# Optimization experiments

Hardware: AMD Instinct MI355X
Metric: run time of the kernel (lower is better)

## Reference

```python
import jax, jax.numpy as jnp
import numpy as np

B, S, HID = 2, 2048, 2048
H, HKV, DH = 32, 8, 64
GROUPS = H // HKV
SCALE = DH ** -0.5
ROPE_THETA = 10000.0
NEG_INF = jnp.finfo(jnp.float32).min


def setup_inputs() -> dict:
    key = jax.random.key(0)
    ks = jax.random.split(key, 6)
    hidden_states = jax.random.normal(ks[0], (B, S, HID), dtype=jnp.float32)
    # true rotary embeddings (HF Llama style): inv_freq over half dim, duplicated
    inv_freq = 1.0 / (ROPE_THETA ** (np.arange(0, DH, 2, dtype=np.float32) / DH))
    freqs = np.arange(S, dtype=np.float32)[:, None] * inv_freq[None, :]  # [S, DH/2]
    emb = np.concatenate([freqs, freqs], axis=-1)                        # [S, DH]
    cos = jnp.broadcast_to(jnp.asarray(np.cos(emb), jnp.float32), (B, S, DH))
    sin = jnp.broadcast_to(jnp.asarray(np.sin(emb), jnp.float32), (B, S, DH))
    # additive causal mask [1,1,S,S]
    causal = jnp.tril(jnp.ones((S, S), dtype=bool))
    attention_mask = jnp.where(causal, 0.0, NEG_INF)[None, None].astype(jnp.float32)
    std = 0.02
    Wq = jax.random.normal(ks[1], (H * DH, HID), dtype=jnp.float32) * std
    Wk = jax.random.normal(ks[2], (HKV * DH, HID), dtype=jnp.float32) * std
    Wv = jax.random.normal(ks[3], (HKV * DH, HID), dtype=jnp.float32) * std
    Wo = jax.random.normal(ks[4], (HID, H * DH), dtype=jnp.float32) * std
    return {"hidden_states": hidden_states, "cos": cos, "sin": sin,
            "attention_mask": attention_mask, "Wq": Wq, "Wk": Wk, "Wv": Wv, "Wo": Wo}


def _rotate_half(x):
    x1, x2 = jnp.split(x, 2, axis=-1)
    return jnp.concatenate([-x2, x1], axis=-1)


def reference(hidden_states, cos, sin, attention_mask, Wq, Wk, Wv, Wo):
    b, s, _ = hidden_states.shape
    # projections -> [B, H(kv), S, DH]
    q = (hidden_states @ Wq.T).reshape(b, s, H, DH).transpose(0, 2, 1, 3)
    k = (hidden_states @ Wk.T).reshape(b, s, HKV, DH).transpose(0, 2, 1, 3)
    v = (hidden_states @ Wv.T).reshape(b, s, HKV, DH).transpose(0, 2, 1, 3)
    # RoPE (cos/sin: [B,S,DH] -> broadcast over head axis)
    c = cos[:, None, :, :]
    sn = sin[:, None, :, :]
    q = q * c + _rotate_half(q) * sn
    k = k * c + _rotate_half(k) * sn
    # GQA: repeat kv heads
    k = jnp.repeat(k, GROUPS, axis=1)  # [B,H,S,DH]
    v = jnp.repeat(v, GROUPS, axis=1)
    # eager attention: full [B,H,S,S] scores in memory
    scores = jnp.einsum('bhqd,bhkd->bhqk', q, k) * SCALE + attention_mask[:, :, :, :s]
    attn = jax.nn.softmax(scores, axis=-1)
    out = jnp.einsum('bhqk,bhkd->bhqd', attn, v)
    out = out.transpose(0, 2, 1, 3).reshape(b, s, H * DH)
    return out @ Wo.T
```

## Files before the change

### kernel.cpp

```cpp
#include <hip/hip_runtime.h>
#include <hip/hip_bf16.h>
#include <cstdint>
#include <cstddef>

#define B_    2
#define S_    2048
#define HID_  2048
#define H_    32
#define HKV_  8
#define DH_   64
#define SC2_  0.1803368801111244f

typedef __bf16 bf16;
typedef bf16  bf16x2 __attribute__((ext_vector_type(2)));
typedef bf16  bf16x4 __attribute__((ext_vector_type(4)));
typedef bf16  bf16x8 __attribute__((ext_vector_type(8)));
typedef float f32x4  __attribute__((ext_vector_type(4)));
typedef float f32x16 __attribute__((ext_vector_type(16)));
typedef uint32_t u32x2 __attribute__((ext_vector_type(2)));

typedef __attribute__((address_space(3))) uint32_t  lds_u32_t;
typedef __attribute__((address_space(1))) const uint32_t glob_u32_t;

__device__ __forceinline__ void async16(const void* g, void* l) {
    __builtin_amdgcn_global_load_lds((glob_u32_t*)g, (lds_u32_t*)l, 16, 0, 0);
}

__device__ __forceinline__ bf16x8 cvt8(float4 a, float4 b) {
    bf16x8 r;
    r[0] = (bf16)a.x; r[1] = (bf16)a.y; r[2] = (bf16)a.z; r[3] = (bf16)a.w;
    r[4] = (bf16)b.x; r[5] = (bf16)b.y; r[6] = (bf16)b.z; r[7] = (bf16)b.w;
    return r;
}

__device__ __forceinline__ uint32_t pkbf(float a, float b) {
    bf16x2 t; t[0] = (bf16)a; t[1] = (bf16)b;
    return __builtin_bit_cast(uint32_t, t);
}
__device__ __forceinline__ bf16x8 mk8(uint32_t a, uint32_t b, uint32_t c, uint32_t d) {
    union { uint32_t u[4]; bf16x8 v; } t;
    t.u[0] = a; t.u[1] = b; t.u[2] = c; t.u[3] = d;
    return t.v;
}

__global__ __launch_bounds__(256) void cvt_all_kernel(
    const float* __restrict__ X,  const float* __restrict__ Wq,
    const float* __restrict__ Wk, const float* __restrict__ Wv,
    const float* __restrict__ Wo,
    bf16* __restrict__ Xb,  bf16* __restrict__ Wqb, bf16* __restrict__ Wkb,
    bf16* __restrict__ Wvb, bf16* __restrict__ Wob)
{
    const int i = blockIdx.x * 256 + threadIdx.x;
    const float* src; bf16* dst; int off;
    if (i < 1048576)      { src = X;  dst = Xb;  off = i; }
    else if (i < 1572864) { src = Wq; dst = Wqb; off = i - 1048576; }
    else if (i < 1703936) { src = Wk; dst = Wkb; off = i - 1572864; }
    else if (i < 1835008) { src = Wv; dst = Wvb; off = i - 1703936; }
    else                  { src = Wo; dst = Wob; off = i - 1835008; }
    float4 a = ((const float4*)src)[2 * off];
    float4 b = ((const float4*)src)[2 * off + 1];
    ((bf16x8*)dst)[off] = cvt8(a, b);
}

__global__ __launch_bounds__(256) void gemm_qkv_kernel(
    const bf16* __restrict__ A,
    const bf16* __restrict__ Wqb, const bf16* __restrict__ Wkb,
    const bf16* __restrict__ Wvb,
    const float* __restrict__ cs, const float* __restrict__ sn,
    bf16* __restrict__ Qo, bf16* __restrict__ Ko, bf16* __restrict__ Vt)
{
    __shared__ bf16 a_lds[2][128 * 64];
    __shared__ bf16 b_lds[2][128 * 64];

    const int tid  = threadIdx.x;
    const int wave = tid >> 6;
    const int lane = tid & 63;
    const int quad = lane >> 4;
    const int l16  = lane & 15;
    const int wm   = wave >> 1;
    const int wn   = wave & 1;

    const int idx = blockIdx.x + 32 * blockIdx.y;
    const int swz = (idx & 7) * 96 + (idx >> 3);
    const int m0  = (swz & 31) * 128;
    const int n0  = (swz >> 5) * 128;

    f32x4 acc[4][4];
    #pragma unroll
    for (int mt = 0; mt < 4; ++mt)
        #pragma unroll
        for (int nt = 0; nt < 4; ++nt)
            acc[mt][nt] = (f32x4){0.f, 0.f, 0.f, 0.f};

    int srow[4], sgcol[4];
    const bf16* browp[4];
    #pragma unroll
    for (int i = 0; i < 4; ++i) {
        const int e = tid * 8 + i * 2048;
        srow[i] = e >> 6;
        const int chunk = (e >> 3) & 7;
        sgcol[i] = (chunk ^ (srow[i] & 7)) << 3;
        const int n = n0 + srow[i];
        browp[i] = (n < 2048) ? (Wqb + (size_t)n * HID_)
                 : (n < 2560) ? (Wkb + (size_t)(n - 2048) * HID_)
                              : (Wvb + (size_t)(n - 2560) * HID_);
    }

    #pragma unroll
    for (int i = 0; i < 4; ++i) {
        async16(A + (size_t)(m0 + srow[i]) * HID_ + sgcol[i],
                &a_lds[0][tid * 8 + i * 2048]);
        async16(browp[i] + sgcol[i],
                &b_lds[0][tid * 8 + i * 2048]);
    }
    __syncthreads();

    for (int k0 = 0; k0 < HID_; k0 += 64) {
        const int cur = (k0 >> 6) & 1;
        if (k0 + 64 < HID_) {
            #pragma unroll
            for (int i = 0; i < 4; ++i) {
                async16(A + (size_t)(m0 + srow[i]) * HID_ + k0 + 64 + sgcol[i],
                        &a_lds[cur ^ 1][tid * 8 + i * 2048]);
                async16(browp[i] + k0 + 64 + sgcol[i],
                        &b_lds[cur ^ 1][tid * 8 + i * 2048]);
            }
        }
        const bf16* al = a_lds[cur];
        const bf16* bl = b_lds[cur];
        #pragma unroll
        for (int ks = 0; ks < 2; ++ks) {
            bf16x8 af[4], bfr[4];
            #pragma unroll
            for (int mt = 0; mt < 4; ++mt) {
                const int row = wm * 64 + mt * 16 + l16;
                const int c = (ks * 4 + quad) ^ (row & 7);
                af[mt] = *(const bf16x8*)(&al[row * 64 + c * 8]);
            }
            #pragma unroll
            for (int nt = 0; nt < 4; ++nt) {
                const int row = wn * 64 + nt * 16 + l16;
                const int c = (ks * 4 + quad) ^ (row & 7);
                bfr[nt] = *(const bf16x8*)(&bl[row * 64 + c * 8]);
            }
            #pragma unroll
            for (int mt = 0; mt < 4; ++mt)
                #pragma unroll
                for (int nt = 0; nt < 4; ++nt)
                    acc[mt][nt] = __builtin_amdgcn_mfma_f32_16x16x32_bf16(
                        af[mt], bfr[nt], acc[mt][nt], 0, 0, 0);
        }
        __syncthreads();
    }

    const int nw = n0 + wn * 64;
    const int d  = l16;
    #pragma unroll
    for (int mt = 0; mt < 4; ++mt) {
        #pragma unroll
        for (int r = 0; r < 4; ++r) {
            const int m  = m0 + wm * 64 + mt * 16 + quad * 4 + r;
            const int bb = m >> 11;
            const int ss = m & (S_ - 1);
            const float v0 = acc[mt][0][r], v1 = acc[mt][1][r];
            const float v2 = acc[mt][2][r], v3 = acc[mt][3][r];
            if (nw < 2048) {
                const int h = nw >> 6;
                bf16* dp = Qo + ((size_t)(bb * H_ + h) * S_ + ss) * DH_;
                const float* cp = cs + ((size_t)bb * S_ + ss) * DH_;
                const float* sp = sn + ((size_t)bb * S_ + ss) * DH_;
                dp[ 0 + d] = (bf16)((v0 * cp[ 0 + d] - v2 * sp[ 0 + d]) * SC2_);
                dp[16 + d] = (bf16)((v1 * cp[16 + d] - v3 * sp[16 + d]) * SC2_);
                dp[32 + d] = (bf16)((v2 * cp[32 + d] + v0 * sp[32 + d]) * SC2_);
                dp[48 + d] = (bf16)((v3 * cp[48 + d] + v1 * sp[48 + d]) * SC2_);
            } else if (nw < 2560) {
                const int h = (nw - 2048) >> 6;
                bf16* dp = Ko + ((size_t)(bb * HKV_ + h) * S_ + ss) * DH_;
                const float* cp = cs + ((size_t)bb * S_ + ss) * DH_;
                const float* sp = sn + ((size_t)bb * S_ + ss) * DH_;
                dp[ 0 + d] = (bf16)(v0 * cp[ 0 + d] - v2 * sp[ 0 + d]);
                dp[16 + d] = (bf16)(v1 * cp[16 + d] - v3 * sp[16 + d]);
                dp[32 + d] = (bf16)(v2 * cp[32 + d] + v0 * sp[32 + d]);
                dp[48 + d] = (bf16)(v3 * cp[48 + d] + v1 * sp[48 + d]);
            } else {
                const int h = (nw - 2560) >> 6;
                bf16* dp = Vt + ((size_t)(bb * HKV_ + h) * DH_) * S_ + ss;
                dp[(size_t)( 0 + d) * S_] = (bf16)v0;
                dp[(size_t)(16 + d) * S_] = (bf16)v1;
                dp[(size_t)(32 + d) * S_] = (bf16)v2;
                dp[(size_t)(48 + d) * S_] = (bf16)v3;
            }
        }
    }
}

__global__ __launch_bounds__(256) void gemm_out_kernel(
    const bf16* __restrict__ A, const bf16* __restrict__ Wb,
    float* __restrict__ Y)
{
    __shared__ bf16 a_lds[2][128 * 64];
    __shared__ bf16 b_lds[2][128 * 64];

    const int tid  = threadIdx.x;
    const int wave = tid >> 6;
    const int lane = tid & 63;
    const int quad = lane >> 4;
    const int l16  = lane & 15;
    const int wm   = wave >> 1;
    const int wn   = wave & 1;

    const int idx = blockIdx.x + 32 * blockIdx.y;
    const int swz = (idx & 7) * 64 + (idx >> 3);
    const int m0  = (swz & 31) * 128;
    const int n0  = (swz >> 5) * 128;

    f32x4 acc[4][4];
    #pragma unroll
    for (int mt = 0; mt < 4; ++mt)
        #pragma unroll
        for (int nt = 0; nt < 4; ++nt)
            acc[mt][nt] = (f32x4){0.f, 0.f, 0.f, 0.f};

    int srow[4], sgcol[4];
    #pragma unroll
    for (int i = 0; i < 4; ++i) {
        const int e = tid * 8 + i * 2048;
        srow[i] = e >> 6;
        const int chunk = (e >> 3) & 7;
        sgcol[i] = (chunk ^ (srow[i] & 7)) << 3;
    }

    #pragma unroll
    for (int i = 0; i < 4; ++i) {
        async16(A + (size_t)(m0 + srow[i]) * HID_ + sgcol[i],
                &a_lds[0][tid * 8 + i * 2048]);
        async16(Wb + (size_t)(n0 + srow[i]) * HID_ + sgcol[i],
                &b_lds[0][tid * 8 + i * 2048]);
    }
    __syncthreads();

    for (int k0 = 0; k0 < HID_; k0 += 64) {
        const int cur = (k0 >> 6) & 1;
        if (k0 + 64 < HID_) {
            #pragma unroll
            for (int i = 0; i < 4; ++i) {
                async16(A + (size_t)(m0 + srow[i]) * HID_ + k0 + 64 + sgcol[i],
                        &a_lds[cur ^ 1][tid * 8 + i * 2048]);
                async16(Wb + (size_t)(n0 + srow[i]) * HID_ + k0 + 64 + sgcol[i],
                        &b_lds[cur ^ 1][tid * 8 + i * 2048]);
            }
        }
        const bf16* al = a_lds[cur];
        const bf16* bl = b_lds[cur];
        #pragma unroll
        for (int ks = 0; ks < 2; ++ks) {
            bf16x8 af[4], bfr[4];
            #pragma unroll
            for (int mt = 0; mt < 4; ++mt) {
                const int row = wm * 64 + mt * 16 + l16;
                const int c = (ks * 4 + quad) ^ (row & 7);
                af[mt] = *(const bf16x8*)(&al[row * 64 + c * 8]);
            }
            #pragma unroll
            for (int nt = 0; nt < 4; ++nt) {
                const int row = wn * 64 + nt * 16 + l16;
                const int c = (ks * 4 + quad) ^ (row & 7);
                bfr[nt] = *(const bf16x8*)(&bl[row * 64 + c * 8]);
            }
            #pragma unroll
            for (int mt = 0; mt < 4; ++mt)
                #pragma unroll
                for (int nt = 0; nt < 4; ++nt)
                    acc[mt][nt] = __builtin_amdgcn_mfma_f32_16x16x32_bf16(
                        af[mt], bfr[nt], acc[mt][nt], 0, 0, 0);
        }
        __syncthreads();
    }

    #pragma unroll
    for (int mt = 0; mt < 4; ++mt)
        #pragma unroll
        for (int nt = 0; nt < 4; ++nt)
            #pragma unroll
            for (int r = 0; r < 4; ++r) {
                const int m = m0 + wm * 64 + mt * 16 + quad * 4 + r;
                const int n = n0 + wn * 64 + nt * 16 + l16;
                Y[(size_t)m * HID_ + n] = acc[mt][nt][r];
            }
}

__global__ __launch_bounds__(256) void attn_kernel(
    const bf16* __restrict__ Q, const bf16* __restrict__ K,
    const bf16* __restrict__ Vt, bf16* __restrict__ O)
{
    __shared__ bf16 k_lds[2][64 * 64];
    __shared__ bf16 v_lds[2][64 * 64];

    const int tid  = threadIdx.x;
    const int wave = tid >> 6;
    const int lane = tid & 63;
    const int l32  = lane & 31;
    const int half = lane >> 5;
    const int h  = blockIdx.y;
    const int b  = blockIdx.z;
    const int hkv = h >> 2;

    const bf16* Qg = Q  + (size_t)(b * H_ + h) * S_ * DH_;
    const bf16* Kg = K  + (size_t)(b * HKV_ + hkv) * S_ * DH_;
    const bf16* Vg = Vt + ((size_t)(b * HKV_ + hkv) * DH_) * S_;

    const int srow0  = tid >> 3;
    const int scolsw = ((tid & 7) ^ ((tid >> 3) & 7)) << 3;

    #pragma unroll 1
    for (int ph = 0; ph < 2; ++ph) {
        const int qt  = ph == 0 ? (int)blockIdx.x : (15 - (int)blockIdx.x);
        const int q0  = qt * 128;
        const int qb0 = q0 + wave * 32;
        const int qa  = qb0 + l32;

        bf16x8 qf[4];
        #pragma unroll
        for (int c = 0; c < 4; ++c)
            qf[c] = *(const bf16x8*)(Qg + (size_t)qa * DH_ + c * 16 + half * 8);

        f32x16 o_acc[2];
        #pragma unroll
        for (int dt = 0; dt < 2; ++dt)
            #pragma unroll
            for (int e = 0; e < 16; ++e) o_acc[dt][e] = 0.f;
        float m_i = -1e30f, l_i = 0.f;

        const int nkt = 2 * qt + 2;

        #pragma unroll
        for (int i = 0; i < 2; ++i) {
            const int row = srow0 + i * 32;
            async16(Kg + (size_t)row * DH_ + scolsw, &k_lds[0][tid * 8 + i * 2048]);
            async16(Vg + (size_t)row * S_  + scolsw, &v_lds[0][tid * 8 + i * 2048]);
        }
        __syncthreads();

        for (int kt = 0; kt < nkt; ++kt) {
            if (kt + 1 < nkt) {
                bf16* kb = k_lds[(kt + 1) & 1];
                bf16* vb = v_lds[(kt + 1) & 1];
                #pragma unroll
                for (int i = 0; i < 2; ++i) {
                    const int row = srow0 + i * 32;
                    async16(Kg + (size_t)((kt + 1) * 64 + row) * DH_ + scolsw,
                            kb + tid * 8 + i * 2048);
                    async16(Vg + (size_t)row * S_ + (kt + 1) * 64 + scolsw,
                            vb + tid * 8 + i * 2048);
                }
            }

            if (kt * 64 <= qb0 + 31) {
                const bf16* kb = k_lds[kt & 1];
                const bf16* vb = v_lds[kt & 1];
                const bool act1 = (kt * 64 + 32) <= (qb0 + 31);

                f32x16 s0, s1;
                {
                    bf16x8 kf[4];
                    #pragma unroll
                    for (int c = 0; c < 4; ++c) {
                        const int col = ((2 * c + half) ^ (l32 & 7)) << 3;
                        kf[c] = *(const bf16x8*)(kb + l32 * 64 + col);
                    }
                    f32x16 a;
                    #pragma unroll
                    for (int e = 0; e < 16; ++e) a[e] = 0.f;
                    __builtin_amdgcn_s_setprio(1);
                    #pragma unroll
                    for (int c = 0; c < 4; ++c)
                        a = __builtin_amdgcn_mfma_f32_32x32x16_bf16(kf[c], qf[c], a, 0, 0, 0);
                    __builtin_amdgcn_s_setprio(0);
                    s0 = a;
                }
                if (act1) {
                    bf16x8 kf[4];
                    #pragma unroll
                    for (int c = 0; c < 4; ++c) {
                        const int row = 32 + l32;
                        const int col = ((2 * c + half) ^ (row & 7)) << 3;
                        kf[c] = *(const bf16x8*)(kb + row * 64 + col);
                    }
                    f32x16 a;
                    #pragma unroll
                    for (int e = 0; e < 16; ++e) a[e] = 0.f;
                    __builtin_amdgcn_s_setprio(1);
                    #pragma unroll
                    for (int c = 0; c < 4; ++c)
                        a = __builtin_amdgcn_mfma_f32_32x32x16_bf16(kf[c], qf[c], a, 0, 0, 0);
                    __builtin_amdgcn_s_setprio(0);
                    s1 = a;
                }

                if (!((kt * 64 + 31) <= qb0)) {
                    const int qrel = qa - kt * 64 - 4 * half;
                    #pragma unroll
                    for (int e = 0; e < 16; ++e)
                        if (((e & 3) + 8 * (e >> 2)) > qrel) s0[e] = -1e30f;
                }
                if (act1 && !((kt * 64 + 63) <= qb0)) {
                    const int qrel = qa - kt * 64 - 32 - 4 * half;
                    #pragma unroll
                    for (int e = 0; e < 16; ++e)
                        if (((e & 3) + 8 * (e >> 2)) > qrel) s1[e] = -1e30f;
                }

                float mx = s0[0];
                #pragma unroll
                for (int e = 1; e < 16; ++e) mx = fmaxf(mx, s0[e]);
                if (act1)
                    #pragma unroll
                    for (int e = 0; e < 16; ++e) mx = fmaxf(mx, s1[e]);
                mx = fmaxf(mx, __shfl_xor(mx, 32));

                float al = 1.f;
                if (!__all(mx <= m_i + 8.f)) {
                    const float mn = fmaxf(m_i, mx);
                    al = exp2f(m_i - mn);
                    m_i = mn;
                    #pragma unroll
                    for (int dt = 0; dt < 2; ++dt)
                        #pragma unroll
                        for (int e = 0; e < 16; ++e) o_acc[dt][e] *= al;
                }

                float sm = 0.f;
                #pragma unroll
                for (int e = 0; e < 16; ++e) {
                    const float pp = exp2f(s0[e] - m_i);
                    s0[e] = pp; sm += pp;
                }
                if (act1)
                    #pragma unroll
                    for (int e = 0; e < 16; ++e) {
                        const float pp = exp2f(s1[e] - m_i);
                        s1[e] = pp; sm += pp;
                    }
                sm += __shfl_xor(sm, 32);
                l_i = l_i * al + sm;

                bf16x8 pf[4];
                {
                    uint32_t d0 = pkbf(s0[0],  s0[1]),  d1 = pkbf(s0[2],  s0[3]);
                    uint32_t d2 = pkbf(s0[4],  s0[5]),  d3 = pkbf(s0[6],  s0[7]);
                    uint32_t d4 = pkbf(s0[8],  s0[9]),  d5 = pkbf(s0[10], s0[11]);
                    uint32_t d6 = pkbf(s0[12], s0[13]), d7 = pkbf(s0[14], s0[15]);
                    u32x2 r02 = __builtin_amdgcn_permlane32_swap(d0, d2, false, false);
                    u32x2 r13 = __builtin_amdgcn_permlane32_swap(d1, d3, false, false);
                    u32x2 r46 = __builtin_amdgcn_permlane32_swap(d4, d6, false, false);
                    u32x2 r57 = __builtin_amdgcn_permlane32_swap(d5, d7, false, false);
                    pf[0] = mk8(r02[0], r13[0], r02[1], r13[1]);
                    pf[1] = mk8(r46[0], r57[0], r46[1], r57[1]);
                }
                if (act1) {
                    uint32_t d0 = pkbf(s1[0],  s1[1]),  d1 = pkbf(s1[2],  s1[3]);
                    uint32_t d2 = pkbf(s1[4],  s1[5]),  d3 = pkbf(s1[6],  s1[7]);
                    uint32_t d4 = pkbf(s1[8],  s1[9]),  d5 = pkbf(s1[10], s1[11]);
                    uint32_t d6 = pkbf(s1[12], s1[13]), d7 = pkbf(s1[14], s1[15]);
                    u32x2 r02 = __builtin_amdgcn_permlane32_swap(d0, d2, false, false);
                    u32x2 r13 = __builtin_amdgcn_permlane32_swap(d1, d3, false, false);
                    u32x2 r46 = __builtin_amdgcn_permlane32_swap(d4, d6, false, false);
                    u32x2 r57 = __builtin_amdgcn_permlane32_swap(d5, d7, false, false);
                    pf[2] = mk8(r02[0], r13[0], r02[1], r13[1]);
                    pf[3] = mk8(r46[0], r57[0], r46[1], r57[1]);
                }

                bf16x8 vf[2][4];
                #pragma unroll
                for (int dt = 0; dt < 2; ++dt)
                    #pragma unroll
                    for (int c = 0; c < 4; ++c) {
                        const int row = dt * 32 + l32;
                        const int col = ((2 * c + half) ^ (row & 7)) << 3;
                        vf[dt][c] = *(const bf16x8*)(vb + row * 64 + col);
                    }

                const int nc = act1 ? 4 : 2;
                __builtin_amdgcn_s_setprio(1);
                #pragma unroll
                for (int c = 0; c < 4; ++c) {
                    if (c >= nc) break;
                    #pragma unroll
                    for (int dt = 0; dt < 2; ++dt)
                        o_acc[dt] = __builtin_amdgcn_mfma_f32_32x32x16_bf16(
                            vf[dt][c], pf[c], o_acc[dt], 0, 0, 0);
                }
                __builtin_amdgcn_s_setprio(0);
            }
            __syncthreads();
        }

        const float inv = 1.f / l_i;
        bf16* op = O + ((size_t)(b * S_ + qa) * H_ + h) * DH_;
        #pragma unroll
        for (int dt = 0; dt < 2; ++dt)
            #pragma unroll
            for (int g = 0; g < 4; ++g) {
                bf16x4 ov;
                #pragma unroll
                for (int r = 0; r < 4; ++r) ov[r] = (bf16)(o_acc[dt][g * 4 + r] * inv);
                *(bf16x4*)(op + dt * 32 + g * 8 + half * 4) = ov;
            }
        __syncthreads();
    }
}

extern "C" void kernel_launch(void* const* d_in, const int* in_sizes, int n_in,
                              void* d_out, int out_size, void* d_ws, size_t ws_size,
                              hipStream_t stream)
{
    const float* X    = (const float*)d_in[0];
    const float* cs   = (const float*)d_in[1];
    const float* sn   = (const float*)d_in[2];
    const float* Wq   = (const float*)d_in[4];
    const float* Wk   = (const float*)d_in[5];
    const float* Wv   = (const float*)d_in[6];
    const float* Wo   = (const float*)d_in[7];
    float* Y          = (float*)d_out;

    bf16* Xb  = (bf16*)d_ws;
    bf16* Wqb = Xb  + (size_t)8388608;
    bf16* Wkb = Wqb + (size_t)4194304;
    bf16* Wvb = Wkb + (size_t)1048576;
    bf16* Wob = Wvb + (size_t)1048576;
    bf16* Qb  = Wob + (size_t)4194304;
    bf16* Kb  = Qb  + (size_t)8388608;
    bf16* Vtb = Kb  + (size_t)2097152;
    bf16* Ob  = Vtb + (size_t)2097152;

    dim3 blk(256);
    cvt_all_kernel<<<dim3(9216), blk, 0, stream>>>(X, Wq, Wk, Wv, Wo,
                                                   Xb, Wqb, Wkb, Wvb, Wob);
    gemm_qkv_kernel<<<dim3(32, 24), blk, 0, stream>>>(Xb, Wqb, Wkb, Wvb,
                                                      cs, sn, Qb, Kb, Vtb);
    attn_kernel<<<dim3(8, H_, B_), blk, 0, stream>>>(Qb, Kb, Vtb, Ob);
    gemm_out_kernel<<<dim3(32, 16), blk, 0, stream>>>(Ob, Wob, Y);
}
```

Before: 349.0 us.

## Flatten attention grid to one block per query tile with heavy-first ordering

Replaces the 512-block grid, where each block processed a pair of mirrored causal query tiles, with a 1D grid of 1024 blocks that each handle a single 128-row query tile. Blocks are ordered so the longest causal tiles (largest qt) are dispatched first across all batch-heads, then progressively shorter ones, giving a longest-job-first schedule. The aim is better load balance and more blocks in flight on the 256 CUs. The cost is losing the per-block pairing that evened out work, plus an extra Q load and prologue per tile.

```diff
diff --git a/kernel.cpp b/kernel.cpp
--- a/kernel.cpp
+++ b/kernel.cpp
@@ -301,8 +301,19 @@
     const int lane = tid & 63;
     const int l32  = lane & 31;
     const int half = lane >> 5;
-    const int h  = blockIdx.y;
-    const int b  = blockIdx.z;
+
+    const int j  = blockIdx.x;
+    const int g  = j >> 8;
+    const int p  = j & 255;
+    const int s  = p >> 6;
+    const int bh = p & 63;
+    const int h  = bh & 31;
+    const int b  = bh >> 5;
+    int qt;
+    if      (g == 0) qt = 15 - s;
+    else if (g == 1) qt = 8 + s;
+    else if (g == 2) qt = 7 - s;
+    else             qt = s;
     const int hkv = h >> 2;
 
     const bf16* Qg = Q  + (size_t)(b * H_ + h) * S_ * DH_;
@@ -312,202 +323,195 @@
     const int srow0  = tid >> 3;
     const int scolsw = ((tid & 7) ^ ((tid >> 3) & 7)) << 3;
 
-    #pragma unroll 1
-    for (int ph = 0; ph < 2; ++ph) {
-        const int qt  = ph == 0 ? (int)blockIdx.x : (15 - (int)blockIdx.x);
-        const int q0  = qt * 128;
-        const int qb0 = q0 + wave * 32;
-        const int qa  = qb0 + l32;
-
-        bf16x8 qf[4];
-        #pragma unroll
-        for (int c = 0; c < 4; ++c)
-            qf[c] = *(const bf16x8*)(Qg + (size_t)qa * DH_ + c * 16 + half * 8);
-
-        f32x16 o_acc[2];
-        #pragma unroll
-        for (int dt = 0; dt < 2; ++dt)
-            #pragma unroll
-            for (int e = 0; e < 16; ++e) o_acc[dt][e] = 0.f;
-        float m_i = -1e30f, l_i = 0.f;
-
-        const int nkt = 2 * qt + 2;
-
-        #pragma unroll
-        for (int i = 0; i < 2; ++i) {
-            const int row = srow0 + i * 32;
-            async16(Kg + (size_t)row * DH_ + scolsw, &k_lds[0][tid * 8 + i * 2048]);
-            async16(Vg + (size_t)row * S_  + scolsw, &v_lds[0][tid * 8 + i * 2048]);
-        }
-        __syncthreads();
-
-        for (int kt = 0; kt < nkt; ++kt) {
-            if (kt + 1 < nkt) {
-                bf16* kb = k_lds[(kt + 1) & 1];
-                bf16* vb = v_lds[(kt + 1) & 1];
-                #pragma unroll
-                for (int i = 0; i < 2; ++i) {
-                    const int row = srow0 + i * 32;
-                    async16(Kg + (size_t)((kt + 1) * 64 + row) * DH_ + scolsw,
-                            kb + tid * 8 + i * 2048);
-                    async16(Vg + (size_t)row * S_ + (kt + 1) * 64 + scolsw,
-                            vb + tid * 8 + i * 2048);
+    const int qb0 = qt * 128 + wave * 32;
+    const int qa  = qb0 + l32;
+    const int nkt = 2 * qt + 2;
+
+    bf16x8 qf[4];
+    #pragma unroll
+    for (int c = 0; c < 4; ++c)
+        qf[c] = *(const bf16x8*)(Qg + (size_t)qa * DH_ + c * 16 + half * 8);
+
+    f32x16 o_acc[2];
+    #pragma unroll
+    for (int dt = 0; dt < 2; ++dt)
+        #pragma unroll
+        for (int e = 0; e < 16; ++e) o_acc[dt][e] = 0.f;
+    float m_i = -1e30f, l_i = 0.f;
+
+    #pragma unroll
+    for (int i = 0; i < 2; ++i) {
+        const int row = srow0 + i * 32;
+        async16(Kg + (size_t)row * DH_ + scolsw, &k_lds[0][tid * 8 + i * 2048]);
+        async16(Vg + (size_t)row * S_  + scolsw, &v_lds[0][tid * 8 + i * 2048]);
+    }
+    __syncthreads();
+
+    for (int kt = 0; kt < nkt; ++kt) {
+        if (kt + 1 < nkt) {
+            bf16* kb = k_lds[(kt + 1) & 1];
+            bf16* vb = v_lds[(kt + 1) & 1];
+            #pragma unroll
+            for (int i = 0; i < 2; ++i) {
+                const int row = srow0 + i * 32;
+                async16(Kg + (size_t)((kt + 1) * 64 + row) * DH_ + scolsw,
+                        kb + tid * 8 + i * 2048);
+                async16(Vg + (size_t)row * S_ + (kt + 1) * 64 + scolsw,
+                        vb + tid * 8 + i * 2048);
+            }
+        }
+
+        if (kt * 64 <= qb0 + 31) {
+            const bf16* kb = k_lds[kt & 1];
+            const bf16* vb = v_lds[kt & 1];
+            const bool act1 = (kt * 64 + 32) <= (qb0 + 31);
+
+            f32x16 s0, s1;
+            {
+                bf16x8 kf[4];
+                #pragma unroll
+                for (int c = 0; c < 4; ++c) {
+                    const int col = ((2 * c + half) ^ (l32 & 7)) << 3;
+                    kf[c] = *(const bf16x8*)(kb + l32 * 64 + col);
                 }
-            }
-
-            if (kt * 64 <= qb0 + 31) {
-                const bf16* kb = k_lds[kt & 1];
-                const bf16* vb = v_lds[kt & 1];
-                const bool act1 = (kt * 64 + 32) <= (qb0 + 31);
-
-                f32x16 s0, s1;
-                {
-                    bf16x8 kf[4];
-                    #pragma unroll
-                    for (int c = 0; c < 4; ++c) {
-                        const int col = ((2 * c + half) ^ (l32 & 7)) << 3;
-                        kf[c] = *(const bf16x8*)(kb + l32 * 64 + col);
-                    }
-                    f32x16 a;
-                    #pragma unroll
-                    for (int e = 0; e < 16; ++e) a[e] = 0.f;
-                    __builtin_amdgcn_s_setprio(1);
-                    #pragma unroll
-                    for (int c = 0; c < 4; ++c)
-                        a = __builtin_amdgcn_mfma_f32_32x32x16_bf16(kf[c], qf[c], a, 0, 0, 0);
-                    __builtin_amdgcn_s_setprio(0);
-                    s0 = a;
+                f32x16 a;
+                #pragma unroll
+                for (int e = 0; e < 16; ++e) a[e] = 0.f;
+                __builtin_amdgcn_s_setprio(1);
+                #pragma unroll
+                for (int c = 0; c < 4; ++c)
+                    a = __builtin_amdgcn_mfma_f32_32x32x16_bf16(kf[c], qf[c], a, 0, 0, 0);
+                __builtin_amdgcn_s_setprio(0);
+                s0 = a;
+            }
+            if (act1) {
+                bf16x8 kf[4];
+                #pragma unroll
+                for (int c = 0; c < 4; ++c) {
+                    const int row = 32 + l32;
+                    const int col = ((2 * c + half) ^ (row & 7)) << 3;
+                    kf[c] = *(const bf16x8*)(kb + row * 64 + col);
                 }
-                if (act1) {
-                    bf16x8 kf[4];
-                    #pragma unroll
-                    for (int c = 0; c < 4; ++c) {
-                        const int row = 32 + l32;
-                        const int col = ((2 * c + half) ^ (row & 7)) << 3;
-                        kf[c] = *(const bf16x8*)(kb + row * 64 + col);
-                    }
-                    f32x16 a;
-                    #pragma unroll
-                    for (int e = 0; e < 16; ++e) a[e] = 0.f;
-                    __builtin_amdgcn_s_setprio(1);
-                    #pragma unroll
-                    for (int c = 0; c < 4; ++c)
-                        a = __builtin_amdgcn_mfma_f32_32x32x16_bf16(kf[c], qf[c], a, 0, 0, 0);
-                    __builtin_amdgcn_s_setprio(0);
-                    s1 = a;
-                }
-
-                if (!((kt * 64 + 31) <= qb0)) {
-                    const int qrel = qa - kt * 64 - 4 * half;
-                    #pragma unroll
-                    for (int e = 0; e < 16; ++e)
-                        if (((e & 3) + 8 * (e >> 2)) > qrel) s0[e] = -1e30f;
-                }
-                if (act1 && !((kt * 64 + 63) <= qb0)) {
-                    const int qrel = qa - kt * 64 - 32 - 4 * half;
-                    #pragma unroll
-                    for (int e = 0; e < 16; ++e)
-                        if (((e & 3) + 8 * (e >> 2)) > qrel) s1[e] = -1e30f;
-                }
-
-                float mx = s0[0];
-                #pragma unroll
-                for (int e = 1; e < 16; ++e) mx = fmaxf(mx, s0[e]);
-                if (act1)
-                    #pragma unroll
-                    for (int e = 0; e < 16; ++e) mx = fmaxf(mx, s1[e]);
-                mx = fmaxf(mx, __shfl_xor(mx, 32));
-
-                float al = 1.f;
-                if (!__all(mx <= m_i + 8.f)) {
-                    const float mn = fmaxf(m_i, mx);
-                    al = exp2f(m_i - mn);
-                    m_i = mn;
-                    #pragma unroll
-                    for (int dt = 0; dt < 2; ++dt)
-                        #pragma unroll
-                        for (int e = 0; e < 16; ++e) o_acc[dt][e] *= al;
-                }
-
-                float sm = 0.f;
-                #pragma unroll
-                for (int e = 0; e < 16; ++e) {
-                    const float pp = exp2f(s0[e] - m_i);
-                    s0[e] = pp; sm += pp;
-                }
-                if (act1)
-                    #pragma unroll
-                    for (int e = 0; e < 16; ++e) {
-                        const float pp = exp2f(s1[e] - m_i);
-                        s1[e] = pp; sm += pp;
-                    }
-                sm += __shfl_xor(sm, 32);
-                l_i = l_i * al + sm;
-
-                bf16x8 pf[4];
-                {
-                    uint32_t d0 = pkbf(s0[0],  s0[1]),  d1 = pkbf(s0[2],  s0[3]);
-                    uint32_t d2 = pkbf(s0[4],  s0[5]),  d3 = pkbf(s0[6],  s0[7]);
-                    uint32_t d4 = pkbf(s0[8],  s0[9]),  d5 = pkbf(s0[10], s0[11]);
-                    uint32_t d6 = pkbf(s0[12], s0[13]), d7 = pkbf(s0[14], s0[15]);
-                    u32x2 r02 = __builtin_amdgcn_permlane32_swap(d0, d2, false, false);
-                    u32x2 r13 = __builtin_amdgcn_permlane32_swap(d1, d3, false, false);
-                    u32x2 r46 = __builtin_amdgcn_permlane32_swap(d4, d6, false, false);
-                    u32x2 r57 = __builtin_amdgcn_permlane32_swap(d5, d7, false, false);
-                    pf[0] = mk8(r02[0], r13[0], r02[1], r13[1]);
-                    pf[1] = mk8(r46[0], r57[0], r46[1], r57[1]);
-                }
-                if (act1) {
-                    uint32_t d0 = pkbf(s1[0],  s1[1]),  d1 = pkbf(s1[2],  s1[3]);
-                    uint32_t d2 = pkbf(s1[4],  s1[5]),  d3 = pkbf(s1[6],  s1[7]);
-                    uint32_t d4 = pkbf(s1[8],  s1[9]),  d5 = pkbf(s1[10], s1[11]);
-                    uint32_t d6 = pkbf(s1[12], s1[13]), d7 = pkbf(s1[14], s1[15]);
-                    u32x2 r02 = __builtin_amdgcn_permlane32_swap(d0, d2, false, false);
-                    u32x2 r13 = __builtin_amdgcn_permlane32_swap(d1, d3, false, false);
-                    u32x2 r46 = __builtin_amdgcn_permlane32_swap(d4, d6, false, false);
-                    u32x2 r57 = __builtin_amdgcn_permlane32_swap(d5, d7, false, false);
-                    pf[2] = mk8(r02[0], r13[0], r02[1], r13[1]);
-                    pf[3] = mk8(r46[0], r57[0], r46[1], r57[1]);
-                }
-
-                bf16x8 vf[2][4];
+                f32x16 a;
+                #pragma unroll
+                for (int e = 0; e < 16; ++e) a[e] = 0.f;
+                __builtin_amdgcn_s_setprio(1);
+                #pragma unroll
+                for (int c = 0; c < 4; ++c)
+                    a = __builtin_amdgcn_mfma_f32_32x32x16_bf16(kf[c], qf[c], a, 0, 0, 0);
+                __builtin_amdgcn_s_setprio(0);
+                s1 = a;
+            }
+
+            if (!((kt * 64 + 31) <= qb0)) {
+                const int qrel = qa - kt * 64 - 4 * half;
+                #pragma unroll
+                for (int e = 0; e < 16; ++e)
+                    if (((e & 3) + 8 * (e >> 2)) > qrel) s0[e] = -1e30f;
+            }
+            if (act1 && !((kt * 64 + 63) <= qb0)) {
+                const int qrel = qa - kt * 64 - 32 - 4 * half;
+                #pragma unroll
+                for (int e = 0; e < 16; ++e)
+                    if (((e & 3) + 8 * (e >> 2)) > qrel) s1[e] = -1e30f;
+            }
+
+            float mx = s0[0];
+            #pragma unroll
+            for (int e = 1; e < 16; ++e) mx = fmaxf(mx, s0[e]);
+            if (act1)
+                #pragma unroll
+                for (int e = 0; e < 16; ++e) mx = fmaxf(mx, s1[e]);
+            mx = fmaxf(mx, __shfl_xor(mx, 32));
+
+            float al = 1.f;
+            if (!__all(mx <= m_i + 8.f)) {
+                const float mn = fmaxf(m_i, mx);
+                al = exp2f(m_i - mn);
+                m_i = mn;
                 #pragma unroll
                 for (int dt = 0; dt < 2; ++dt)
                     #pragma unroll
-                    for (int c = 0; c < 4; ++c) {
-                        const int row = dt * 32 + l32;
-                        const int col = ((2 * c + half) ^ (row & 7)) << 3;
-                        vf[dt][c] = *(const bf16x8*)(vb + row * 64 + col);
-                    }
-
-                const int nc = act1 ? 4 : 2;
-                __builtin_amdgcn_s_setprio(1);
+                    for (int e = 0; e < 16; ++e) o_acc[dt][e] *= al;
+            }
+
+            float sm = 0.f;
+            #pragma unroll
+            for (int e = 0; e < 16; ++e) {
+                const float pp = exp2f(s0[e] - m_i);
+                s0[e] = pp; sm += pp;
+            }
+            if (act1)
+                #pragma unroll
+                for (int e = 0; e < 16; ++e) {
+                    const float pp = exp2f(s1[e] - m_i);
+                    s1[e] = pp; sm += pp;
+                }
+            sm += __shfl_xor(sm, 32);
+            l_i = l_i * al + sm;
+
+            bf16x8 pf[4];
+            {
+                uint32_t d0 = pkbf(s0[0],  s0[1]),  d1 = pkbf(s0[2],  s0[3]);
+                uint32_t d2 = pkbf(s0[4],  s0[5]),  d3 = pkbf(s0[6],  s0[7]);
+                uint32_t d4 = pkbf(s0[8],  s0[9]),  d5 = pkbf(s0[10], s0[11]);
+                uint32_t d6 = pkbf(s0[12], s0[13]), d7 = pkbf(s0[14], s0[15]);
+                u32x2 r02 = __builtin_amdgcn_permlane32_swap(d0, d2, false, false);
+                u32x2 r13 = __builtin_amdgcn_permlane32_swap(d1, d3, false, false);
+                u32x2 r46 = __builtin_amdgcn_permlane32_swap(d4, d6, false, false);
+                u32x2 r57 = __builtin_amdgcn_permlane32_swap(d5, d7, false, false);
+                pf[0] = mk8(r02[0], r13[0], r02[1], r13[1]);
+                pf[1] = mk8(r46[0], r57[0], r46[1], r57[1]);
+            }
+            if (act1) {
+                uint32_t d0 = pkbf(s1[0],  s1[1]),  d1 = pkbf(s1[2],  s1[3]);
+                uint32_t d2 = pkbf(s1[4],  s1[5]),  d3 = pkbf(s1[6],  s1[7]);
+                uint32_t d4 = pkbf(s1[8],  s1[9]),  d5 = pkbf(s1[10], s1[11]);
+                uint32_t d6 = pkbf(s1[12], s1[13]), d7 = pkbf(s1[14], s1[15]);
+                u32x2 r02 = __builtin_amdgcn_permlane32_swap(d0, d2, false, false);
+                u32x2 r13 = __builtin_amdgcn_permlane32_swap(d1, d3, false, false);
+                u32x2 r46 = __builtin_amdgcn_permlane32_swap(d4, d6, false, false);
+                u32x2 r57 = __builtin_amdgcn_permlane32_swap(d5, d7, false, false);
+                pf[2] = mk8(r02[0], r13[0], r02[1], r13[1]);
+                pf[3] = mk8(r46[0], r57[0], r46[1], r57[1]);
+            }
+
+            bf16x8 vf[2][4];
+            #pragma unroll
+            for (int dt = 0; dt < 2; ++dt)
                 #pragma unroll
                 for (int c = 0; c < 4; ++c) {
-                    if (c >= nc) break;
-                    #pragma unroll
-                    for (int dt = 0; dt < 2; ++dt)
-                        o_acc[dt] = __builtin_amdgcn_mfma_f32_32x32x16_bf16(
-                            vf[dt][c], pf[c], o_acc[dt], 0, 0, 0);
+                    const int row = dt * 32 + l32;
+                    const int col = ((2 * c + half) ^ (row & 7)) << 3;
+                    vf[dt][c] = *(const bf16x8*)(vb + row * 64 + col);
                 }
-                __builtin_amdgcn_s_setprio(0);
-            }
-            __syncthreads();
-        }
-
-        const float inv = 1.f / l_i;
-        bf16* op = O + ((size_t)(b * S_ + qa) * H_ + h) * DH_;
-        #pragma unroll
-        for (int dt = 0; dt < 2; ++dt)
-            #pragma unroll
-            for (int g = 0; g < 4; ++g) {
-                bf16x4 ov;
-                #pragma unroll
-                for (int r = 0; r < 4; ++r) ov[r] = (bf16)(o_acc[dt][g * 4 + r] * inv);
-                *(bf16x4*)(op + dt * 32 + g * 8 + half * 4) = ov;
-            }
+
+            const int nc = act1 ? 4 : 2;
+            __builtin_amdgcn_s_setprio(1);
+            #pragma unroll
+            for (int c = 0; c < 4; ++c) {
+                if (c >= nc) break;
+                #pragma unroll
+                for (int dt = 0; dt < 2; ++dt)
+                    o_acc[dt] = __builtin_amdgcn_mfma_f32_32x32x16_bf16(
+                        vf[dt][c], pf[c], o_acc[dt], 0, 0, 0);
+            }
+            __builtin_amdgcn_s_setprio(0);
+        }
         __syncthreads();
     }
+
+    const float inv = 1.f / l_i;
+    bf16* op = O + ((size_t)(b * S_ + qa) * H_ + h) * DH_;
+    #pragma unroll
+    for (int dt = 0; dt < 2; ++dt)
+        #pragma unroll
+        for (int g2 = 0; g2 < 4; ++g2) {
+            bf16x4 ov;
+            #pragma unroll
+            for (int r = 0; r < 4; ++r) ov[r] = (bf16)(o_acc[dt][g2 * 4 + r] * inv);
+            *(bf16x4*)(op + dt * 32 + g2 * 8 + half * 4) = ov;
+        }
 }
 
 extern "C" void kernel_launch(void* const* d_in, const int* in_sizes, int n_in,
@@ -538,6 +542,6 @@
                                                    Xb, Wqb, Wkb, Wvb, Wob);
     gemm_qkv_kernel<<<dim3(32, 24), blk, 0, stream>>>(Xb, Wqb, Wkb, Wvb,
                                                       cs, sn, Qb, Kb, Vtb);
-    attn_kernel<<<dim3(8, H_, B_), blk, 0, stream>>>(Qb, Kb, Vtb, Ob);
+    attn_kernel<<<dim3(1024), blk, 0, stream>>>(Qb, Kb, Vtb, Ob);
     gemm_out_kernel<<<dim3(32, 16), blk, 0, stream>>>(Ob, Wob, Y);
 }
```

New measurement: 350.3 us. Within noise of the previous version (+0.4%).

## Enlarge QKV GEMM to 256x256 tiles with 8 waves and interleaved staging

Applied to the files above, without the earlier changes.

The QKV projection GEMM moves from 128x128 tiles with 4 waves to 256x256 tiles with 8 waves. Each wave computes four 64x32 quadrant sub-tiles. The K loop is restructured into phases separated by barriers, and the next tile's A and B loads are issued between MFMA groups under an explicit vmcnt wait. s_setprio is raised around the MFMA bursts. The goal is more operand reuse per byte loaded and better overlap of global loads with matrix math. The grid shrinks to 192 blocks, which may underfill the 256 CUs, and LDS use doubles to 128KB per block.

```diff
diff --git a/kernel.cpp b/kernel.cpp
--- a/kernel.cpp
+++ b/kernel.cpp
@@ -62,133 +62,212 @@
     ((bf16x8*)dst)[off] = cvt8(a, b);
 }
 
-__global__ __launch_bounds__(256) void gemm_qkv_kernel(
+__global__ __launch_bounds__(512) void gemm_qkv_kernel(
     const bf16* __restrict__ A,
     const bf16* __restrict__ Wqb, const bf16* __restrict__ Wkb,
     const bf16* __restrict__ Wvb,
     const float* __restrict__ cs, const float* __restrict__ sn,
     bf16* __restrict__ Qo, bf16* __restrict__ Ko, bf16* __restrict__ Vt)
 {
-    __shared__ bf16 a_lds[2][128 * 64];
-    __shared__ bf16 b_lds[2][128 * 64];
+    __shared__ bf16 a_lds[2][2][128 * 64];
+    __shared__ bf16 b_lds[2][2][128 * 64];
 
     const int tid  = threadIdx.x;
     const int wave = tid >> 6;
     const int lane = tid & 63;
     const int quad = lane >> 4;
     const int l16  = lane & 15;
-    const int wm   = wave >> 1;
-    const int wn   = wave & 1;
-
-    const int idx = blockIdx.x + 32 * blockIdx.y;
-    const int swz = (idx & 7) * 96 + (idx >> 3);
-    const int m0  = (swz & 31) * 128;
-    const int n0  = (swz >> 5) * 128;
-
-    f32x4 acc[4][4];
+    const int wm   = wave >> 2;
+    const int wn   = wave & 3;
+    const int bh   = wn >> 1;
+
+    const int idx = blockIdx.x + 16 * blockIdx.y;
+    const int swz = (idx & 7) * 24 + (idx >> 3);
+    const int m0  = (swz & 15) * 256;
+    const int n0  = (swz >> 4) * 256;
+
+    int srow[2], sgcol[2];
+    const bf16* browp[2][2];
     #pragma unroll
-    for (int mt = 0; mt < 4; ++mt)
-        #pragma unroll
-        for (int nt = 0; nt < 4; ++nt)
-            acc[mt][nt] = (f32x4){0.f, 0.f, 0.f, 0.f};
-
-    int srow[4], sgcol[4];
-    const bf16* browp[4];
-    #pragma unroll
-    for (int i = 0; i < 4; ++i) {
-        const int e = tid * 8 + i * 2048;
+    for (int i = 0; i < 2; ++i) {
+        const int e = tid * 8 + i * 4096;
         srow[i] = e >> 6;
         const int chunk = (e >> 3) & 7;
         sgcol[i] = (chunk ^ (srow[i] & 7)) << 3;
-        const int n = n0 + srow[i];
-        browp[i] = (n < 2048) ? (Wqb + (size_t)n * HID_)
-                 : (n < 2560) ? (Wkb + (size_t)(n - 2048) * HID_)
-                              : (Wvb + (size_t)(n - 2560) * HID_);
+        #pragma unroll
+        for (int h = 0; h < 2; ++h) {
+            const int n = n0 + h * 128 + srow[i];
+            browp[h][i] = (n < 2048) ? (Wqb + (size_t)n * HID_)
+                        : (n < 2560) ? (Wkb + (size_t)(n - 2048) * HID_)
+                                     : (Wvb + (size_t)(n - 2560) * HID_);
+        }
     }
 
+    auto stageA = [&](int u) {
+        const int k0 = u * 64;
+        #pragma unroll
+        for (int h = 0; h < 2; ++h)
+            #pragma unroll
+            for (int i = 0; i < 2; ++i)
+                async16(A + (size_t)(m0 + h * 128 + srow[i]) * HID_ + k0 + sgcol[i],
+                        &a_lds[u & 1][h][tid * 8 + i * 4096]);
+    };
+    auto stageB = [&](int u) {
+        const int k0 = u * 64;
+        #pragma unroll
+        for (int h = 0; h < 2; ++h)
+            #pragma unroll
+            for (int i = 0; i < 2; ++i)
+                async16(browp[h][i] + k0 + sgcol[i],
+                        &b_lds[u & 1][h][tid * 8 + i * 4096]);
+    };
+
+    f32x4 acc[2][2][4][2];
     #pragma unroll
-    for (int i = 0; i < 4; ++i) {
-        async16(A + (size_t)(m0 + srow[i]) * HID_ + sgcol[i],
-                &a_lds[0][tid * 8 + i * 2048]);
-        async16(browp[i] + sgcol[i],
-                &b_lds[0][tid * 8 + i * 2048]);
-    }
-    __syncthreads();
-
-    for (int k0 = 0; k0 < HID_; k0 += 64) {
-        const int cur = (k0 >> 6) & 1;
-        if (k0 + 64 < HID_) {
-            #pragma unroll
-            for (int i = 0; i < 4; ++i) {
-                async16(A + (size_t)(m0 + srow[i]) * HID_ + k0 + 64 + sgcol[i],
-                        &a_lds[cur ^ 1][tid * 8 + i * 2048]);
-                async16(browp[i] + k0 + 64 + sgcol[i],
-                        &b_lds[cur ^ 1][tid * 8 + i * 2048]);
-            }
-        }
-        const bf16* al = a_lds[cur];
-        const bf16* bl = b_lds[cur];
-        #pragma unroll
-        for (int ks = 0; ks < 2; ++ks) {
-            bf16x8 af[4], bfr[4];
-            #pragma unroll
-            for (int mt = 0; mt < 4; ++mt) {
-                const int row = wm * 64 + mt * 16 + l16;
+    for (int mq = 0; mq < 2; ++mq)
+        #pragma unroll
+        for (int nq = 0; nq < 2; ++nq)
+            #pragma unroll
+            for (int mt = 0; mt < 4; ++mt)
+                #pragma unroll
+                for (int nt = 0; nt < 2; ++nt)
+                    acc[mq][nq][mt][nt] = (f32x4){0.f, 0.f, 0.f, 0.f};
+
+    stageA(0); stageB(0);
+    stageA(1); stageB(1);
+
+    bf16x8 af[4][2], b0f[2][2], b1f[2][2];
+
+    for (int u = 0; u < 32; ++u) {
+        if (u + 1 < 32) { asm volatile("s_waitcnt vmcnt(8)" ::: "memory"); }
+        else            { asm volatile("s_waitcnt vmcnt(0)" ::: "memory"); }
+        __builtin_amdgcn_s_barrier();
+        __builtin_amdgcn_sched_barrier(0);
+
+        const bf16* al = &a_lds[u & 1][wm][0];
+        const bf16* bl = &b_lds[u & 1][bh][0];
+
+        #pragma unroll
+        for (int mt = 0; mt < 4; ++mt)
+            #pragma unroll
+            for (int ks = 0; ks < 2; ++ks) {
+                const int row = mt * 16 + l16;
                 const int c = (ks * 4 + quad) ^ (row & 7);
-                af[mt] = *(const bf16x8*)(&al[row * 64 + c * 8]);
-            }
-            #pragma unroll
-            for (int nt = 0; nt < 4; ++nt) {
-                const int row = wn * 64 + nt * 16 + l16;
+                af[mt][ks] = *(const bf16x8*)(al + row * 64 + c * 8);
+            }
+        #pragma unroll
+        for (int nt = 0; nt < 2; ++nt)
+            #pragma unroll
+            for (int ks = 0; ks < 2; ++ks) {
+                const int r = (wn & 1) * 64 + nt * 16 + l16;
+                const int c = (ks * 4 + quad) ^ (r & 7);
+                b0f[nt][ks] = *(const bf16x8*)(bl + r * 64 + c * 8);
+            }
+        __builtin_amdgcn_s_setprio(1);
+        #pragma unroll
+        for (int mt = 0; mt < 4; ++mt)
+            #pragma unroll
+            for (int nt = 0; nt < 2; ++nt)
+                #pragma unroll
+                for (int ks = 0; ks < 2; ++ks)
+                    acc[0][0][mt][nt] = __builtin_amdgcn_mfma_f32_16x16x32_bf16(
+                        af[mt][ks], b0f[nt][ks], acc[0][0][mt][nt], 0, 0, 0);
+        __builtin_amdgcn_s_setprio(0);
+        __builtin_amdgcn_s_barrier();
+
+        #pragma unroll
+        for (int nt = 0; nt < 2; ++nt)
+            #pragma unroll
+            for (int ks = 0; ks < 2; ++ks) {
+                const int r = (wn & 1) * 64 + 32 + nt * 16 + l16;
+                const int c = (ks * 4 + quad) ^ (r & 7);
+                b1f[nt][ks] = *(const bf16x8*)(bl + r * 64 + c * 8);
+            }
+        __builtin_amdgcn_s_setprio(1);
+        #pragma unroll
+        for (int mt = 0; mt < 4; ++mt)
+            #pragma unroll
+            for (int nt = 0; nt < 2; ++nt)
+                #pragma unroll
+                for (int ks = 0; ks < 2; ++ks)
+                    acc[0][1][mt][nt] = __builtin_amdgcn_mfma_f32_16x16x32_bf16(
+                        af[mt][ks], b1f[nt][ks], acc[0][1][mt][nt], 0, 0, 0);
+        __builtin_amdgcn_s_setprio(0);
+        __builtin_amdgcn_s_barrier();
+
+        if (u + 2 < 32) stageB(u + 2);
+        #pragma unroll
+        for (int mt = 0; mt < 4; ++mt)
+            #pragma unroll
+            for (int ks = 0; ks < 2; ++ks) {
+                const int row = 64 + mt * 16 + l16;
                 const int c = (ks * 4 + quad) ^ (row & 7);
-                bfr[nt] = *(const bf16x8*)(&bl[row * 64 + c * 8]);
-            }
-            #pragma unroll
-            for (int mt = 0; mt < 4; ++mt)
-                #pragma unroll
-                for (int nt = 0; nt < 4; ++nt)
-                    acc[mt][nt] = __builtin_amdgcn_mfma_f32_16x16x32_bf16(
-                        af[mt], bfr[nt], acc[mt][nt], 0, 0, 0);
-        }
-        __syncthreads();
+                af[mt][ks] = *(const bf16x8*)(al + row * 64 + c * 8);
+            }
+        __builtin_amdgcn_s_setprio(1);
+        #pragma unroll
+        for (int mt = 0; mt < 4; ++mt)
+            #pragma unroll
+            for (int nt = 0; nt < 2; ++nt)
+                #pragma unroll
+                for (int ks = 0; ks < 2; ++ks)
+                    acc[1][1][mt][nt] = __builtin_amdgcn_mfma_f32_16x16x32_bf16(
+                        af[mt][ks], b1f[nt][ks], acc[1][1][mt][nt], 0, 0, 0);
+        __builtin_amdgcn_s_setprio(0);
+        __builtin_amdgcn_s_barrier();
+
+        if (u + 2 < 32) stageA(u + 2);
+        __builtin_amdgcn_s_setprio(1);
+        #pragma unroll
+        for (int mt = 0; mt < 4; ++mt)
+            #pragma unroll
+            for (int nt = 0; nt < 2; ++nt)
+                #pragma unroll
+                for (int ks = 0; ks < 2; ++ks)
+                    acc[1][0][mt][nt] = __builtin_amdgcn_mfma_f32_16x16x32_bf16(
+                        af[mt][ks], b0f[nt][ks], acc[1][0][mt][nt], 0, 0, 0);
+        __builtin_amdgcn_s_setprio(0);
     }
 
     const int nw = n0 + wn * 64;
     const int d  = l16;
     #pragma unroll
-    for (int mt = 0; mt < 4; ++mt) {
-        #pragma unroll
-        for (int r = 0; r < 4; ++r) {
-            const int m  = m0 + wm * 64 + mt * 16 + quad * 4 + r;
-            const int bb = m >> 11;
-            const int ss = m & (S_ - 1);
-            const float v0 = acc[mt][0][r], v1 = acc[mt][1][r];
-            const float v2 = acc[mt][2][r], v3 = acc[mt][3][r];
-            if (nw < 2048) {
-                const int h = nw >> 6;
-                bf16* dp = Qo + ((size_t)(bb * H_ + h) * S_ + ss) * DH_;
-                const float* cp = cs + ((size_t)bb * S_ + ss) * DH_;
-                const float* sp = sn + ((size_t)bb * S_ + ss) * DH_;
-                dp[ 0 + d] = (bf16)((v0 * cp[ 0 + d] - v2 * sp[ 0 + d]) * SC2_);
-                dp[16 + d] = (bf16)((v1 * cp[16 + d] - v3 * sp[16 + d]) * SC2_);
-                dp[32 + d] = (bf16)((v2 * cp[32 + d] + v0 * sp[32 + d]) * SC2_);
-                dp[48 + d] = (bf16)((v3 * cp[48 + d] + v1 * sp[48 + d]) * SC2_);
-            } else if (nw < 2560) {
-                const int h = (nw - 2048) >> 6;
-                bf16* dp = Ko + ((size_t)(bb * HKV_ + h) * S_ + ss) * DH_;
-                const float* cp = cs + ((size_t)bb * S_ + ss) * DH_;
-                const float* sp = sn + ((size_t)bb * S_ + ss) * DH_;
-                dp[ 0 + d] = (bf16)(v0 * cp[ 0 + d] - v2 * sp[ 0 + d]);
-                dp[16 + d] = (bf16)(v1 * cp[16 + d] - v3 * sp[16 + d]);
-                dp[32 + d] = (bf16)(v2 * cp[32 + d] + v0 * sp[32 + d]);
-                dp[48 + d] = (bf16)(v3 * cp[48 + d] + v1 * sp[48 + d]);
-            } else {
-                const int h = (nw - 2560) >> 6;
-                bf16* dp = Vt + ((size_t)(bb * HKV_ + h) * DH_) * S_ + ss;
-                dp[(size_t)( 0 + d) * S_] = (bf16)v0;
-                dp[(size_t)(16 + d) * S_] = (bf16)v1;
-                dp[(size_t)(32 + d) * S_] = (bf16)v2;
-                dp[(size_t)(48 + d) * S_] = (bf16)v3;
+    for (int mq = 0; mq < 2; ++mq) {
+        #pragma unroll
+        for (int mt = 0; mt < 4; ++mt) {
+            #pragma unroll
+            for (int r = 0; r < 4; ++r) {
+                const int m  = m0 + wm * 128 + mq * 64 + mt * 16 + quad * 4 + r;
+                const int bb = m >> 11;
+                const int ss = m & (S_ - 1);
+                const float v0 = acc[mq][0][mt][0][r], v1 = acc[mq][0][mt][1][r];
+                const float v2 = acc[mq][1][mt][0][r], v3 = acc[mq][1][mt][1][r];
+                if (nw < 2048) {
+                    const int h = nw >> 6;
+                    bf16* dp = Qo + ((size_t)(bb * H_ + h) * S_ + ss) * DH_;
+                    const float* cp = cs + ((size_t)bb * S_ + ss) * DH_;
+                    const float* sp = sn + ((size_t)bb * S_ + ss) * DH_;
+                    dp[ 0 + d] = (bf16)((v0 * cp[ 0 + d] - v2 * sp[ 0 + d]) * SC2_);
+                    dp[16 + d] = (bf16)((v1 * cp[16 + d] - v3 * sp[16 + d]) * SC2_);
+                    dp[32 + d] = (bf16)((v2 * cp[32 + d] + v0 * sp[32 + d]) * SC2_);
+                    dp[48 + d] = (bf16)((v3 * cp[48 + d] + v1 * sp[48 + d]) * SC2_);
+                } else if (nw < 2560) {
+                    const int h = (nw - 2048) >> 6;
+                    bf16* dp = Ko + ((size_t)(bb * HKV_ + h) * S_ + ss) * DH_;
+                    const float* cp = cs + ((size_t)bb * S_ + ss) * DH_;
+                    const float* sp = sn + ((size_t)bb * S_ + ss) * DH_;
+                    dp[ 0 + d] = (bf16)(v0 * cp[ 0 + d] - v2 * sp[ 0 + d]);
+                    dp[16 + d] = (bf16)(v1 * cp[16 + d] - v3 * sp[16 + d]);
+                    dp[32 + d] = (bf16)(v2 * cp[32 + d] + v0 * sp[32 + d]);
+                    dp[48 + d] = (bf16)(v3 * cp[48 + d] + v1 * sp[48 + d]);
+                } else {
+                    const int h = (nw - 2560) >> 6;
+                    bf16* dp = Vt + ((size_t)(bb * HKV_ + h) * DH_) * S_ + ss;
+                    dp[(size_t)( 0 + d) * S_] = (bf16)v0;
+                    dp[(size_t)(16 + d) * S_] = (bf16)v1;
+                    dp[(size_t)(32 + d) * S_] = (bf16)v2;
+                    dp[(size_t)(48 + d) * S_] = (bf16)v3;
+                }
             }
         }
     }
@@ -536,8 +615,8 @@
     dim3 blk(256);
     cvt_all_kernel<<<dim3(9216), blk, 0, stream>>>(X, Wq, Wk, Wv, Wo,
                                                    Xb, Wqb, Wkb, Wvb, Wob);
-    gemm_qkv_kernel<<<dim3(32, 24), blk, 0, stream>>>(Xb, Wqb, Wkb, Wvb,
-                                                      cs, sn, Qb, Kb, Vtb);
+    gemm_qkv_kernel<<<dim3(16, 12), dim3(512), 0, stream>>>(Xb, Wqb, Wkb, Wvb,
+                                                            cs, sn, Qb, Kb, Vtb);
     attn_kernel<<<dim3(8, H_, B_), blk, 0, stream>>>(Qb, Kb, Vtb, Ob);
     gemm_out_kernel<<<dim3(32, 16), blk, 0, stream>>>(Ob, Wob, Y);
 }
```

Measured after the change: 352.0 us. Within noise of the previous version (+0.9%).
